# Optimization experiments

Measured on AMD Instinct MI355X. Metric: run time of the kernel, lower is better.

The kernel has to match this reference:

```python
import jax, jax.numpy as jnp
import numpy as np

# DiffeqSolver with method='rk4', adjoint=False: fixed-step classical RK4,
# one step per consecutive pair in time_steps (torchdiffeq fixed-grid behavior).
# ode_func: dy/dt = tanh(y @ W1 + b1) @ W2 + b2 (time-autonomous latent-ODE MLP).

B, D, H, T = 1024, 512, 1024, 64

def setup_inputs() -> dict:
    key = jax.random.key(0)
    k1, k2, k3 = jax.random.split(key, 3)
    first_point = jax.random.normal(k1, (B, D), dtype=jnp.float32)
    time_steps = jnp.linspace(0.0, 1.0, T, dtype=jnp.float32)
    W1 = jax.random.normal(k2, (D, H), dtype=jnp.float32) / np.sqrt(D)
    b1 = jnp.zeros((H,), dtype=jnp.float32)
    W2 = jax.random.normal(k3, (H, D), dtype=jnp.float32) / np.sqrt(H)
    b2 = jnp.zeros((D,), dtype=jnp.float32)
    return {"first_point": first_point, "time_steps": time_steps,
            "W1": W1, "b1": b1, "W2": W2, "b2": b2}


def reference(first_point, time_steps, W1, b1, W2, b2):
    def f(y):  # ode_func(t, y); autonomous
        return jnp.tanh(y @ W1 + b1) @ W2 + b2

    def rk4_step(y, dt):
        half = dt * 0.5
        k1 = f(y)
        k2 = f(y + half * k1)
        k3 = f(y + half * k2)
        k4 = f(y + dt * k3)
        y_next = y + (dt / 6.0) * (k1 + 2.0 * k2 + 2.0 * k3 + k4)
        return y_next, y_next

    dts = time_steps[1:] - time_steps[:-1]  # [T-1]
    _, ys = jax.lax.scan(rk4_step, first_point, dts)
    # odeint returns the solution at every time in time_steps, including t[0]
    pred_y = jnp.concatenate([first_point[None], ys], axis=0)  # [T, B, D]
    return pred_y
```

## Files before the change

kernel.cpp:

```cpp
#include <hip/hip_runtime.h>
#include <hip/hip_bf16.h>


#define B_ 1024
#define D_ 512
#define H_ 1024
#define T_ 64
#define M_ 16
#define NW 16

typedef unsigned short ushort_t;
typedef _Float16 f16x8 __attribute__((ext_vector_type(8)));
typedef float f32x4 __attribute__((ext_vector_type(4)));
typedef unsigned short ushortx8 __attribute__((ext_vector_type(8)));

__device__ __forceinline__ float bf2f(ushort_t u) {
  union { unsigned u; float f; } v;
  v.u = ((unsigned)u) << 16;
  return v.f;
}

__device__ __forceinline__ ushort_t f2h(float f) {
  return __builtin_bit_cast(ushort_t, (_Float16)f);
}

__device__ __forceinline__ float ldf(const void* p, int i, bool f32) {
  return f32 ? ((const float*)p)[i] : bf2f(((const ushort_t*)p)[i]);
}

__device__ __forceinline__ bool is_f32_inputs(const void* ts) {
  return ((const ushort_t*)ts)[1] == 0;
}

__device__ __forceinline__ float tanh_fast(float x) {
  float e = __builtin_amdgcn_exp2f(x * 2.885390081777927f);
  return 1.0f - 2.0f * __builtin_amdgcn_rcpf(e + 1.0f);
}

__device__ __forceinline__ f16x8 ld8(const ushort_t* p) {
  return __builtin_bit_cast(f16x8, *(const ushortx8*)p);
}

__device__ __forceinline__ f32x4 mfma16f(f16x8 a, f16x8 b, f32x4 c) {
  return __builtin_amdgcn_mfma_f32_16x16x32_f16(a, b, c, 0, 0, 0);
}

__global__ void pack_w1(const void* __restrict__ in, ushort_t* __restrict__ out,
                        const void* __restrict__ ts) {
  const bool f32 = is_f32_inputs(ts);
  const int tid = blockIdx.x * blockDim.x + threadIdx.x;
  const int l = tid & 63;
  const int n = (tid >> 6) & 3;
  const int t = (tid >> 8) & 15;
  const int w = tid >> 12;
  const int m = l & 15, q = l >> 4;
  const int c  = w * 64 + n * 16 + m;
  const int kb = t * 32 + q * 8;
  ushortx8 v;
#pragma unroll
  for (int j = 0; j < 8; j++)
    v[j] = f2h(ldf(in, (size_t)(kb + j) * H_ + c, f32));
  *(ushortx8*)(out + (size_t)tid * 8) = v;
}

__global__ void pack_w2(const void* __restrict__ in, ushort_t* __restrict__ out,
                        const void* __restrict__ ts) {
  const bool f32 = is_f32_inputs(ts);
  const int tid = blockIdx.x * blockDim.x + threadIdx.x;
  const int l = tid & 63;
  const int u = (tid >> 6) & 3;
  const int t = (tid >> 8) & 15;
  const int w = tid >> 12;
  const int n = u >> 1, h = u & 1;
  const int m = l & 15, q = l >> 4;
  const int c  = w * 32 + n * 16 + m;
  const int kb = t * 64 + h * 32 + q * 8;
  ushortx8 v;
#pragma unroll
  for (int j = 0; j < 8; j++)
    v[j] = f2h(ldf(in, (size_t)(kb + j) * D_ + c, f32));
  *(ushortx8*)(out + (size_t)tid * 8) = v;
}

__global__ __launch_bounds__(1024, 4)
void rk4_kernel(const void* __restrict__ y0,
                const void* __restrict__ ts,
                const ushort_t* __restrict__ w1f,
                const void* __restrict__ b1,
                const ushort_t* __restrict__ w2f,
                const void* __restrict__ b2,
                float* __restrict__ out)
{
  __shared__ __align__(16) ushort_t yS[M_][D_ + 8];
  __shared__ __align__(16) ushort_t hS[M_][H_ + 8];

  const bool f32i = is_f32_inputs(ts);
  const int tid  = threadIdx.x;
  const int wave = tid >> 6;
  const int lane = tid & 63;
  const int m    = lane & 15;
  const int quad = lane >> 4;
  const int rowbase = blockIdx.x * M_;
  const int cw1 = wave * 64;
  const int cw2 = wave * 32;

  float b1v[4], b2v[2];
#pragma unroll
  for (int n = 0; n < 4; n++) b1v[n] = ldf(b1, cw1 + n * 16 + m, f32i);
#pragma unroll
  for (int n = 0; n < 2; n++) b2v[n] = ldf(b2, cw2 + n * 16 + m, f32i);

  const ushort_t* q1 = w1f + ((size_t)wave << 15) + lane * 8;
  const ushort_t* q2 = w2f + ((size_t)wave << 15) + lane * 8;

  float y[2][4], acc[2][4], k[2][4];
#pragma unroll
  for (int n = 0; n < 2; n++)
#pragma unroll
    for (int r = 0; r < 4; r++) {
      const int row = rowbase + quad * 4 + r;
      const int col = cw2 + n * 16 + m;
      y[n][r] = ldf(y0, row * D_ + col, f32i);
      out[(size_t)row * D_ + col] = y[n][r];
      k[n][r] = 0.0f;
      acc[n][r] = 0.0f;
    }

#pragma unroll 1
  for (int step = 0; step < T_ - 1; step++) {
    const float dt = ldf(ts, step + 1, f32i) - ldf(ts, step, f32i);

#pragma unroll 1
    for (int e = 0; e < 4; e++) {
      const float c = (e == 0) ? 0.0f : ((e == 3) ? dt : 0.5f * dt);
      const float w = ((e == 1) || (e == 2)) ? 2.0f : 1.0f;

#pragma unroll
      for (int n = 0; n < 2; n++)
#pragma unroll
        for (int r = 0; r < 4; r++)
          yS[quad * 4 + r][cw2 + n * 16 + m] = f2h(y[n][r] + c * k[n][r]);
      __syncthreads();

      f32x4 hacc[4];
#pragma unroll
      for (int n = 0; n < 4; n++) hacc[n] = (f32x4){0.f, 0.f, 0.f, 0.f};
      f16x8 a0 = ld8(&yS[m][quad * 8]);
      f16x8 bb[4];
#pragma unroll
      for (int n = 0; n < 4; n++) bb[n] = ld8(q1 + n * 512);
#pragma unroll 1
      for (int t = 0; t < 16; t++) {
        const int tn = (t + 1 < 16) ? (t + 1) : 0;
        f16x8 a1 = ld8(&yS[m][tn * 32 + quad * 8]);
        f16x8 bn[4];
#pragma unroll
        for (int n = 0; n < 4; n++) bn[n] = ld8(q1 + tn * 2048 + n * 512);
#pragma unroll
        for (int n = 0; n < 4; n++) hacc[n] = mfma16f(a0, bb[n], hacc[n]);
        a0 = a1;
#pragma unroll
        for (int n = 0; n < 4; n++) bb[n] = bn[n];
      }

#pragma unroll
      for (int n = 0; n < 4; n++)
#pragma unroll
        for (int r = 0; r < 4; r++)
          hS[quad * 4 + r][cw1 + n * 16 + m] = f2h(tanh_fast(hacc[n][r] + b1v[n]));
      __syncthreads();

      f32x4 kacc[2];
#pragma unroll
      for (int n = 0; n < 2; n++) kacc[n] = (f32x4){0.f, 0.f, 0.f, 0.f};
      f16x8 c0 = ld8(&hS[m][quad * 8]);
      f16x8 c1 = ld8(&hS[m][32 + quad * 8]);
      f16x8 db[4];
#pragma unroll
      for (int u = 0; u < 4; u++) db[u] = ld8(q2 + u * 512);
#pragma unroll 1
      for (int t = 0; t < 16; t++) {
        const int tn = (t + 1 < 16) ? (t + 1) : 0;
        f16x8 a1 = ld8(&hS[m][tn * 64 + quad * 8]);
        f16x8 a2 = ld8(&hS[m][tn * 64 + 32 + quad * 8]);
        f16x8 dn[4];
#pragma unroll
        for (int u = 0; u < 4; u++) dn[u] = ld8(q2 + tn * 2048 + u * 512);
#pragma unroll
        for (int n = 0; n < 2; n++) {
          kacc[n] = mfma16f(c0, db[n * 2], kacc[n]);
          kacc[n] = mfma16f(c1, db[n * 2 + 1], kacc[n]);
        }
        c0 = a1; c1 = a2;
#pragma unroll
        for (int u = 0; u < 4; u++) db[u] = dn[u];
      }

#pragma unroll
      for (int n = 0; n < 2; n++)
#pragma unroll
        for (int r = 0; r < 4; r++) {
          k[n][r] = kacc[n][r] + b2v[n];
          if (e == 0) acc[n][r] = k[n][r];
          else        acc[n][r] += w * k[n][r];
        }
    }

    float* op = out + (size_t)(step + 1) * B_ * D_;
    const float s = dt * (1.0f / 6.0f);
#pragma unroll
    for (int n = 0; n < 2; n++)
#pragma unroll
      for (int r = 0; r < 4; r++) {
        y[n][r] += s * acc[n][r];
        op[(size_t)(rowbase + quad * 4 + r) * D_ + cw2 + n * 16 + m] = y[n][r];
      }
  }
}

extern "C" void kernel_launch(void* const* d_in, const int* in_sizes, int n_in,
                              void* d_out, int out_size, void* d_ws, size_t ws_size,
                              hipStream_t stream) {
  int iTs = -1, sc = 1;
  for (int i = 0; i < n_in; i++)
    if (in_sizes[i] == 64 || in_sizes[i] == 128 || in_sizes[i] == 256) {
      iTs = i; sc = in_sizes[i] / 64; break;
    }
  if (iTs < 0) { iTs = 1; sc = 1; }
  int iB1 = -1, iB2 = -1, bigs[3]; int nb = 0;
  for (int i = 0; i < n_in; i++) {
    if (i == iTs) continue;
    if (in_sizes[i] == 1024 * sc) iB1 = i;
    else if (in_sizes[i] == 512 * sc) iB2 = i;
    else if (nb < 3) bigs[nb++] = i;
  }
  if (iB1 < 0) iB1 = 3;
  if (iB2 < 0) iB2 = 5;
  if (nb < 3) { bigs[0] = 0; bigs[1] = 2; bigs[2] = 4; }
  const void *y0, *w1, *w2;
  if (iTs == 1) {
    y0 = d_in[bigs[0]]; w1 = d_in[bigs[1]]; w2 = d_in[bigs[2]];
  } else {
    w1 = d_in[bigs[0]]; w2 = d_in[bigs[1]]; y0 = d_in[bigs[2]];
  }
  const void* ts = d_in[iTs];
  const void* b1 = d_in[iB1];
  const void* b2 = d_in[iB2];
  float* out = (float*)d_out;

  ushort_t* w1f = (ushort_t*)d_ws;
  ushort_t* w2f = w1f + (size_t)D_ * H_;

  pack_w1<<<dim3(256), dim3(256), 0, stream>>>(w1, w1f, ts);
  pack_w2<<<dim3(256), dim3(256), 0, stream>>>(w2, w2f, ts);

  rk4_kernel<<<dim3(B_ / M_), dim3(1024), 0, stream>>>(y0, ts, w1f, b1, w2f, b2, out);
}
```

Before: 4.028 ms.

## Split hidden dimension across four cooperating blocks with flag-synchronized partial sums

```diff
diff --git a/kernel.cpp b/kernel.cpp
--- a/kernel.cpp
+++ b/kernel.cpp
@@ -7,7 +7,6 @@
 #define H_ 1024
 #define T_ 64
 #define M_ 16
-#define NW 16
 
 typedef unsigned short ushort_t;
 typedef _Float16 f16x8 __attribute__((ext_vector_type(8)));
@@ -50,16 +49,15 @@
   const bool f32 = is_f32_inputs(ts);
   const int tid = blockIdx.x * blockDim.x + threadIdx.x;
   const int l = tid & 63;
-  const int n = (tid >> 6) & 3;
-  const int t = (tid >> 8) & 15;
-  const int w = tid >> 12;
-  const int m = l & 15, q = l >> 4;
-  const int c  = w * 64 + n * 16 + m;
-  const int kb = t * 32 + q * 8;
+  const int t = (tid >> 6) & 15;
+  const int w = (tid >> 10) & 15;
+  const int q = (tid >> 14) & 3;
+  const int col = q * 256 + w * 16 + (l & 15);
+  const int kb  = t * 32 + (l >> 4) * 8;
   ushortx8 v;
 #pragma unroll
   for (int j = 0; j < 8; j++)
-    v[j] = f2h(ldf(in, (size_t)(kb + j) * H_ + c, f32));
+    v[j] = f2h(ldf(in, (size_t)(kb + j) * H_ + col, f32));
   *(ushortx8*)(out + (size_t)tid * 8) = v;
 }
 
@@ -68,31 +66,32 @@
   const bool f32 = is_f32_inputs(ts);
   const int tid = blockIdx.x * blockDim.x + threadIdx.x;
   const int l = tid & 63;
-  const int u = (tid >> 6) & 3;
-  const int t = (tid >> 8) & 15;
-  const int w = tid >> 12;
-  const int n = u >> 1, h = u & 1;
-  const int m = l & 15, q = l >> 4;
-  const int c  = w * 32 + n * 16 + m;
-  const int kb = t * 64 + h * 32 + q * 8;
+  const int n = (tid >> 6) & 1;
+  const int t = (tid >> 7) & 7;
+  const int w = (tid >> 10) & 15;
+  const int q = (tid >> 14) & 3;
+  const int col = w * 32 + n * 16 + (l & 15);
+  const int kb  = q * 256 + t * 32 + (l >> 4) * 8;
   ushortx8 v;
 #pragma unroll
   for (int j = 0; j < 8; j++)
-    v[j] = f2h(ldf(in, (size_t)(kb + j) * D_ + c, f32));
+    v[j] = f2h(ldf(in, (size_t)(kb + j) * D_ + col, f32));
   *(ushortx8*)(out + (size_t)tid * 8) = v;
 }
 
 __global__ __launch_bounds__(1024, 4)
 void rk4_kernel(const void* __restrict__ y0,
                 const void* __restrict__ ts,
-                const ushort_t* __restrict__ w1f,
+                const ushort_t* __restrict__ w1p,
                 const void* __restrict__ b1,
-                const ushort_t* __restrict__ w2f,
+                const ushort_t* __restrict__ w2p,
                 const void* __restrict__ b2,
+                float* __restrict__ part,
+                unsigned int* __restrict__ flags,
                 float* __restrict__ out)
 {
   __shared__ __align__(16) ushort_t yS[M_][D_ + 8];
-  __shared__ __align__(16) ushort_t hS[M_][H_ + 8];
+  __shared__ __align__(16) ushort_t hS[M_][256 + 8];
 
   const bool f32i = is_f32_inputs(ts);
   const int tid  = threadIdx.x;
@@ -100,18 +99,20 @@
   const int lane = tid & 63;
   const int m    = lane & 15;
   const int quad = lane >> 4;
-  const int rowbase = blockIdx.x * M_;
-  const int cw1 = wave * 64;
+  const int bid  = blockIdx.x;
+  const int q    = (bid >> 3) & 3;
+  const int rg   = (bid & 7) + ((bid >> 5) << 3);
+  const int rowbase = rg * M_;
   const int cw2 = wave * 32;
 
-  float b1v[4], b2v[2];
-#pragma unroll
-  for (int n = 0; n < 4; n++) b1v[n] = ldf(b1, cw1 + n * 16 + m, f32i);
+  const float b1v = ldf(b1, q * 256 + wave * 16 + m, f32i);
+  float b2v[2];
 #pragma unroll
   for (int n = 0; n < 2; n++) b2v[n] = ldf(b2, cw2 + n * 16 + m, f32i);
 
-  const ushort_t* q1 = w1f + ((size_t)wave << 15) + lane * 8;
-  const ushort_t* q2 = w2f + ((size_t)wave << 15) + lane * 8;
+  const ushort_t* q1 = w1p + ((size_t)(q * 16 + wave) << 13) + lane * 8;
+  const ushort_t* q2 = w2p + ((size_t)(q * 16 + wave) << 13) + lane * 8;
+  unsigned int* myflag = flags + ((rg * 4 + q) << 4);
 
   float y[2][4], acc[2][4], k[2][4];
 #pragma unroll
@@ -121,7 +122,7 @@
       const int row = rowbase + quad * 4 + r;
       const int col = cw2 + n * 16 + m;
       y[n][r] = ldf(y0, row * D_ + col, f32i);
-      out[(size_t)row * D_ + col] = y[n][r];
+      if (q == 0) out[(size_t)row * D_ + col] = y[n][r];
       k[n][r] = 0.0f;
       acc[n][r] = 0.0f;
     }
@@ -133,7 +134,9 @@
 #pragma unroll 1
     for (int e = 0; e < 4; e++) {
       const float c = (e == 0) ? 0.0f : ((e == 3) ? dt : 0.5f * dt);
-      const float w = ((e == 1) || (e == 2)) ? 2.0f : 1.0f;
+      const float wgt = ((e == 1) || (e == 2)) ? 2.0f : 1.0f;
+      const int sidx = step * 4 + e;
+      const int par  = sidx & 1;
 
 #pragma unroll
       for (int n = 0; n < 2; n++)
@@ -142,68 +145,81 @@
           yS[quad * 4 + r][cw2 + n * 16 + m] = f2h(y[n][r] + c * k[n][r]);
       __syncthreads();
 
-      f32x4 hacc[4];
-#pragma unroll
-      for (int n = 0; n < 4; n++) hacc[n] = (f32x4){0.f, 0.f, 0.f, 0.f};
+      f32x4 hacc = (f32x4){0.f, 0.f, 0.f, 0.f};
       f16x8 a0 = ld8(&yS[m][quad * 8]);
-      f16x8 bb[4];
-#pragma unroll
-      for (int n = 0; n < 4; n++) bb[n] = ld8(q1 + n * 512);
-#pragma unroll 1
+      f16x8 b0 = ld8(q1);
+#pragma unroll 4
       for (int t = 0; t < 16; t++) {
-        const int tn = (t + 1 < 16) ? (t + 1) : 0;
+        const int tn = (t + 1) & 15;
         f16x8 a1 = ld8(&yS[m][tn * 32 + quad * 8]);
-        f16x8 bn[4];
-#pragma unroll
-        for (int n = 0; n < 4; n++) bn[n] = ld8(q1 + tn * 2048 + n * 512);
-#pragma unroll
-        for (int n = 0; n < 4; n++) hacc[n] = mfma16f(a0, bb[n], hacc[n]);
-        a0 = a1;
-#pragma unroll
-        for (int n = 0; n < 4; n++) bb[n] = bn[n];
-      }
-
-#pragma unroll
-      for (int n = 0; n < 4; n++)
-#pragma unroll
-        for (int r = 0; r < 4; r++)
-          hS[quad * 4 + r][cw1 + n * 16 + m] = f2h(tanh_fast(hacc[n][r] + b1v[n]));
+        f16x8 bn = ld8(q1 + tn * 512);
+        hacc = mfma16f(a0, b0, hacc);
+        a0 = a1; b0 = bn;
+      }
+
+#pragma unroll
+      for (int r = 0; r < 4; r++)
+        hS[quad * 4 + r][wave * 16 + m] = f2h(tanh_fast(hacc[r] + b1v));
       __syncthreads();
 
       f32x4 kacc[2];
 #pragma unroll
       for (int n = 0; n < 2; n++) kacc[n] = (f32x4){0.f, 0.f, 0.f, 0.f};
       f16x8 c0 = ld8(&hS[m][quad * 8]);
-      f16x8 c1 = ld8(&hS[m][32 + quad * 8]);
-      f16x8 db[4];
-#pragma unroll
-      for (int u = 0; u < 4; u++) db[u] = ld8(q2 + u * 512);
-#pragma unroll 1
-      for (int t = 0; t < 16; t++) {
-        const int tn = (t + 1 < 16) ? (t + 1) : 0;
-        f16x8 a1 = ld8(&hS[m][tn * 64 + quad * 8]);
-        f16x8 a2 = ld8(&hS[m][tn * 64 + 32 + quad * 8]);
-        f16x8 dn[4];
-#pragma unroll
-        for (int u = 0; u < 4; u++) dn[u] = ld8(q2 + tn * 2048 + u * 512);
-#pragma unroll
-        for (int n = 0; n < 2; n++) {
-          kacc[n] = mfma16f(c0, db[n * 2], kacc[n]);
-          kacc[n] = mfma16f(c1, db[n * 2 + 1], kacc[n]);
+      f16x8 d0 = ld8(q2);
+      f16x8 d1 = ld8(q2 + 512);
+#pragma unroll 4
+      for (int t = 0; t < 8; t++) {
+        const int tn = (t + 1) & 7;
+        f16x8 a1 = ld8(&hS[m][tn * 32 + quad * 8]);
+        f16x8 e0 = ld8(q2 + tn * 1024);
+        f16x8 e1 = ld8(q2 + tn * 1024 + 512);
+        kacc[0] = mfma16f(c0, d0, kacc[0]);
+        kacc[1] = mfma16f(c0, d1, kacc[1]);
+        c0 = a1; d0 = e0; d1 = e1;
+      }
+
+      {
+        float* pb = part + ((size_t)((par * 64 + rg) * 4 + q) << 13);
+#pragma unroll
+        for (int n = 0; n < 2; n++)
+#pragma unroll
+          for (int r = 0; r < 4; r++)
+            pb[(quad * 4 + r) * 512 + cw2 + n * 16 + m] = kacc[n][r];
+      }
+      __syncthreads();
+      if (tid == 0) {
+        __threadfence();
+        atomicAdd(myflag, 1u);
+      }
+      if (tid < 4 && tid != q) {
+        unsigned int* pf = flags + ((rg * 4 + tid) << 4);
+        const unsigned int tgt = (unsigned int)(sidx + 1);
+        int spins = 0;
+        while (__hip_atomic_load(pf, __ATOMIC_RELAXED, __HIP_MEMORY_SCOPE_AGENT) < tgt) {
+          __builtin_amdgcn_s_sleep(1);
+          if (++spins > (1 << 19)) break;
         }
-        c0 = a1; c1 = a2;
-#pragma unroll
-        for (int u = 0; u < 4; u++) db[u] = dn[u];
-      }
-
-#pragma unroll
-      for (int n = 0; n < 2; n++)
-#pragma unroll
-        for (int r = 0; r < 4; r++) {
-          k[n][r] = kacc[n][r] + b2v[n];
-          if (e == 0) acc[n][r] = k[n][r];
-          else        acc[n][r] += w * k[n][r];
-        }
+        __threadfence();
+      }
+      __syncthreads();
+
+      {
+        const float* pr = part + ((size_t)((par * 64 + rg) * 4) << 13);
+#pragma unroll
+        for (int n = 0; n < 2; n++)
+#pragma unroll
+          for (int r = 0; r < 4; r++) {
+            const size_t eo = (size_t)(quad * 4 + r) * 512 + cw2 + n * 16 + m;
+            float s = b2v[n];
+#pragma unroll
+            for (int qq = 0; qq < 4; qq++)
+              s += (qq == q) ? kacc[n][r] : pr[((size_t)qq << 13) + eo];
+            k[n][r] = s;
+            if (e == 0) acc[n][r] = k[n][r];
+            else        acc[n][r] += wgt * k[n][r];
+          }
+      }
     }
 
     float* op = out + (size_t)(step + 1) * B_ * D_;
@@ -213,7 +229,8 @@
 #pragma unroll
       for (int r = 0; r < 4; r++) {
         y[n][r] += s * acc[n][r];
-        op[(size_t)(rowbase + quad * 4 + r) * D_ + cw2 + n * 16 + m] = y[n][r];
+        if (q == 0)
+          op[(size_t)(rowbase + quad * 4 + r) * D_ + cw2 + n * 16 + m] = y[n][r];
       }
   }
 }
@@ -248,11 +265,17 @@
   const void* b2 = d_in[iB2];
   float* out = (float*)d_out;
 
-  ushort_t* w1f = (ushort_t*)d_ws;
-  ushort_t* w2f = w1f + (size_t)D_ * H_;
-
-  pack_w1<<<dim3(256), dim3(256), 0, stream>>>(w1, w1f, ts);
-  pack_w2<<<dim3(256), dim3(256), 0, stream>>>(w2, w2f, ts);
-
-  rk4_kernel<<<dim3(B_ / M_), dim3(1024), 0, stream>>>(y0, ts, w1f, b1, w2f, b2, out);
-}
+  char* wsb = (char*)d_ws;
+  ushort_t* w1p = (ushort_t*)wsb;
+  ushort_t* w2p = (ushort_t*)(wsb + (1 << 20));
+  unsigned int* flags = (unsigned int*)(wsb + (2 << 20));
+  float* part = (float*)(wsb + (2 << 20) + 16384);
+
+  hipMemsetAsync(flags, 0, 16384, stream);
+
+  pack_w1<<<dim3(256), dim3(256), 0, stream>>>(w1, w1p, ts);
+  pack_w2<<<dim3(256), dim3(256), 0, stream>>>(w2, w2p, ts);
+
+  rk4_kernel<<<dim3(256), dim3(1024), 0, stream>>>(y0, ts, w1p, b1, w2p, b2,
+                                                   part, flags, out);
+}
```

After: 6.263 ms. +55.5%, slower.
